# Kernel optimization log

Measured on AMD Instinct MI355X. Metric: run time of the kernel, lower is better.

Reference implementation:

```python
import jax, jax.numpy as jnp
import numpy as np

B, S, D = 8, 2048, 512
EPS = 1e-6
ROPE_THETA = 10000.0


def setup_inputs() -> dict:
    key = jax.random.key(0)
    ks = jax.random.split(key, 8)
    scale = 0.02
    return {
        "x": jax.random.normal(ks[0], (B, S, D), dtype=jnp.float32),
        "conv_w": jax.random.normal(ks[1], (D, D, 3), dtype=jnp.float32) * scale,
        "conv_b": jnp.zeros((D,), dtype=jnp.float32),
        "pre_g": jnp.ones((D,), dtype=jnp.float32),
        "q_g": jnp.ones((D,), dtype=jnp.float32),
        "k_g": jnp.ones((D,), dtype=jnp.float32),
        "Wq": jax.random.normal(ks[2], (D, D), dtype=jnp.float32) * scale,
        "Wk": jax.random.normal(ks[3], (D, D), dtype=jnp.float32) * scale,
        "Wv": jax.random.normal(ks[4], (D, D), dtype=jnp.float32) * scale,
    }


def _rmsnorm(x, g, eps=EPS):
    ms = jnp.mean(jnp.square(x), axis=-1, keepdims=True)
    return x * jax.lax.rsqrt(ms + eps) * g


def _rope_tables(seq_len, head_dim, dtype=jnp.float32):
    inv = 1.0 / (ROPE_THETA ** (jnp.arange(0, head_dim, 2, dtype=dtype) / head_dim))
    freqs = jnp.arange(seq_len, dtype=dtype)[:, None] * inv[None, :]  # [S, D/2]
    return jnp.cos(freqs), jnp.sin(freqs)


def _apply_rope(x, cos, sin):
    # x: [B, S, D]; treat last dim as D/2 complex pairs (interleaved real/imag)
    b, s, d = x.shape
    xr = x.reshape(b, s, d // 2, 2)
    x0, x1 = xr[..., 0], xr[..., 1]
    c = cos[None, :, :]
    sn = sin[None, :, :]
    o0 = x0 * c - x1 * sn
    o1 = x0 * sn + x1 * c
    return jnp.stack([o0, o1], axis=-1).reshape(b, s, d)


def reference(x, conv_w, conv_b, pre_g, q_g, k_g, Wq, Wk, Wv):
    b, s, d = x.shape
    # Conv1d over sequence axis (kernel 3, padding 1)
    xc = jnp.transpose(x, (0, 2, 1))  # [B, D, S]
    xc = jax.lax.conv_general_dilated(
        xc, conv_w, window_strides=(1,), padding=[(1, 1)],
        dimension_numbers=("NCH", "OIH", "NCH"))
    xc = xc + conv_b[None, :, None]
    x_norm = _rmsnorm(jnp.transpose(xc, (0, 2, 1)), pre_g)  # [B, S, D]

    q = _rmsnorm(jnp.einsum("bsd,ed->bse", x_norm, Wq), q_g)
    k = _rmsnorm(jnp.einsum("bsd,ed->bse", x_norm, Wk), k_g)
    v = jnp.einsum("bsd,ed->bse", x_norm, Wv)

    cos, sin = _rope_tables(s, d, x.dtype)
    q = _apply_rope(q, cos, sin)
    k = _apply_rope(k, cos, sin)

    scores = jnp.einsum("bqd,bkd->bqk", q, k) / jnp.sqrt(jnp.asarray(d, x.dtype))
    w = jax.nn.softmax(scores, axis=-1)  # dropout is identity in eval mode
    attended = jnp.einsum("bqk,bkd->bqd", w, v)
    out = x + attended
    return out.mean(axis=1)  # [B, D]
```

## Files before the change

### kernel.cpp

```cpp
#include <hip/hip_runtime.h>
#include <math.h>

#define BB 8
#define SS 2048
#define DDIM 512
#define KC 1536
#define EPSV 1e-6f
#define SCALE 0.044194173824159216f
#define LDP 40

typedef unsigned short ushort_t;
using short8 = __attribute__((ext_vector_type(8))) short;
using f32x4  = __attribute__((ext_vector_type(4))) float;

__device__ inline unsigned short f2bf(float f) {
    union { float f; unsigned int u; } v; v.f = f;
    unsigned int r = v.u + 0x7FFFu + ((v.u >> 16) & 1u);
    return (unsigned short)(r >> 16);
}
__device__ inline unsigned int packbf(float a, float b) {
    return (unsigned int)f2bf(a) | ((unsigned int)f2bf(b) << 16);
}
__device__ inline float bf2f(unsigned short s) {
    union { unsigned int u; float f; } v; v.u = ((unsigned int)s) << 16; return v.f;
}
__device__ inline short8 ldfrag(const ushort_t* s, int row, int ko) {
    return *reinterpret_cast<const short8*>(&s[row * LDP + ko]);
}

__global__ __launch_bounds__(256) void kx_cast(const float* __restrict__ x, ushort_t* __restrict__ xbf)
{
    int i = (blockIdx.x * 256 + threadIdx.x) * 4;
    float4 v = *reinterpret_cast<const float4*>(&x[i]);
    unsigned int lo = packbf(v.x, v.y), hi = packbf(v.z, v.w);
    *reinterpret_cast<uint2*>(&xbf[i]) = make_uint2(lo, hi);
}

__global__ __launch_bounds__(256) void k0_prep(
    const float* __restrict__ conv_w, const float* __restrict__ Wq,
    const float* __restrict__ Wk, const float* __restrict__ Wv,
    ushort_t* __restrict__ wcat, ushort_t* __restrict__ wqkv)
{
    int idx = blockIdx.x * 256 + threadIdx.x;
    {
        int o = idx / KC, kk = idx - o * KC;
        int t = kk >> 9, i = kk & 511;
        wcat[idx] = f2bf(conv_w[(size_t)o * KC + i * 3 + t]);
    }
    {
        int n = idx >> 9, d = idx & 511;
        const float* src = (n < 512) ? &Wq[(size_t)n * DDIM + d]
                         : (n < 1024) ? &Wk[(size_t)(n - 512) * DDIM + d]
                         : &Wv[(size_t)(n - 1024) * DDIM + d];
        wqkv[idx] = f2bf(*src);
    }
}

__global__ __launch_bounds__(256, 4) void k1b_conv(
    const ushort_t* __restrict__ xbf, const ushort_t* __restrict__ wcat,
    const float* __restrict__ conv_b, ushort_t* __restrict__ ybf, float* __restrict__ rs)
{
    __shared__ ushort_t As[128 * LDP];
    __shared__ ushort_t Bs[128 * LDP];
    const int t = threadIdx.x;
    const int lane = t & 63, w = t >> 6;
    const int lm = lane & 15, lq = lane >> 4;
    const int wm = w >> 1, wn = w & 1;
    const int srow = t >> 2, scol = (t & 3) * 8;
    const int s0 = blockIdx.x * 128;
    const int n0 = blockIdx.y * 128;
    const int b  = blockIdx.z;
    const ushort_t* Ag = xbf + (size_t)b * SS * DDIM;
    const ushort_t* Bg = wcat + (size_t)n0 * KC;

    f32x4 acc[4][4];
    #pragma unroll
    for (int i = 0; i < 4; i++)
        #pragma unroll
        for (int j = 0; j < 4; j++) acc[i][j] = (f32x4){0.f, 0.f, 0.f, 0.f};

    const uint4 z4 = make_uint4(0, 0, 0, 0);
    #define LOADA(dc, ro, dst) { \
        int s_ = s0 + srow + (ro) + ((dc) >> 4) - 1; \
        int ic_ = (((dc) & 15) << 5) + scol; \
        dst = (s_ >= 0 && s_ < SS) ? *reinterpret_cast<const uint4*>(&Ag[(size_t)s_ * DDIM + ic_]) : z4; }

    uint4 ra0, ra1, rb0, rb1;
    LOADA(0, 0, ra0); LOADA(0, 64, ra1);
    rb0 = *reinterpret_cast<const uint4*>(&Bg[(size_t)srow * KC + scol]);
    rb1 = *reinterpret_cast<const uint4*>(&Bg[(size_t)(srow + 64) * KC + scol]);

    for (int dc = 0; dc < 48; dc++) {
        *reinterpret_cast<uint4*>(&As[srow * LDP + scol]) = ra0;
        *reinterpret_cast<uint4*>(&As[(srow + 64) * LDP + scol]) = ra1;
        *reinterpret_cast<uint4*>(&Bs[srow * LDP + scol]) = rb0;
        *reinterpret_cast<uint4*>(&Bs[(srow + 64) * LDP + scol]) = rb1;
        __syncthreads();
        if (dc < 47) {
            LOADA(dc + 1, 0, ra0); LOADA(dc + 1, 64, ra1);
            int c = (dc + 1) * 32 + scol;
            rb0 = *reinterpret_cast<const uint4*>(&Bg[(size_t)srow * KC + c]);
            rb1 = *reinterpret_cast<const uint4*>(&Bg[(size_t)(srow + 64) * KC + c]);
        }
        short8 af[4];
        #pragma unroll
        for (int mt = 0; mt < 4; mt++)
            af[mt] = ldfrag(As, wm * 64 + mt * 16 + lm, lq * 8);
        #pragma unroll
        for (int nt = 0; nt < 4; nt++) {
            short8 bfv = ldfrag(Bs, wn * 64 + nt * 16 + lm, lq * 8);
            #pragma unroll
            for (int mt = 0; mt < 4; mt++)
                acc[mt][nt] = __builtin_amdgcn_mfma_f32_16x16x32_bf16(af[mt], bfv, acc[mt][nt], 0, 0, 0);
        }
        __syncthreads();
    }
    #undef LOADA

    const int rbase = s0 + wm * 64;
    const int cbase = n0 + wn * 64;
    ushort_t* yb = ybf + (size_t)b * SS * DDIM;
    float* rsb = rs + (size_t)b * SS;
    float bias[4];
    #pragma unroll
    for (int nt = 0; nt < 4; nt++) bias[nt] = conv_b[cbase + nt * 16 + lm];
    #pragma unroll
    for (int mt = 0; mt < 4; mt++) {
        float pr[4] = {0.f, 0.f, 0.f, 0.f};
        #pragma unroll
        for (int nt = 0; nt < 4; nt++) {
            #pragma unroll
            for (int r = 0; r < 4; r++) {
                float val = acc[mt][nt][r] + bias[nt];
                yb[(size_t)(rbase + mt * 16 + lq * 4 + r) * DDIM + cbase + nt * 16 + lm] = f2bf(val);
                pr[r] = fmaf(val, val, pr[r]);
            }
        }
        #pragma unroll
        for (int r = 0; r < 4; r++) {
            float p = pr[r];
            p += __shfl_xor(p, 1, 64); p += __shfl_xor(p, 2, 64);
            p += __shfl_xor(p, 4, 64); p += __shfl_xor(p, 8, 64);
            if (lm == 0) atomicAdd(&rsb[rbase + mt * 16 + lq * 4 + r], p);
        }
    }
}

__global__ __launch_bounds__(256) void k1n_norm(
    const ushort_t* __restrict__ ybf, const float* __restrict__ rs,
    const float* __restrict__ pre_g, ushort_t* __restrict__ xnbf)
{
    const int t = threadIdx.x;
    const int b = blockIdx.y;
    const int r0 = blockIdx.x * 8;
    float2 pg = *reinterpret_cast<const float2*>(&pre_g[2 * t]);
    for (int r = 0; r < 8; r++) {
        size_t row = (size_t)b * SS + r0 + r;
        float inv = rsqrtf(rs[row] * (1.0f / DDIM) + EPSV);
        unsigned int yv = *reinterpret_cast<const unsigned int*>(&ybf[row * DDIM + 2 * t]);
        float v0 = bf2f((ushort_t)(yv & 0xFFFF)), v1 = bf2f((ushort_t)(yv >> 16));
        *reinterpret_cast<unsigned int*>(&xnbf[row * DDIM + 2 * t]) =
            packbf(v0 * inv * pg.x, v1 * inv * pg.y);
    }
}

__global__ __launch_bounds__(256, 4) void k1c_qkv(
    const ushort_t* __restrict__ xnbf, const ushort_t* __restrict__ wqkv,
    ushort_t* __restrict__ qraw, ushort_t* __restrict__ kraw, ushort_t* __restrict__ vb,
    float* __restrict__ rq, float* __restrict__ rk)
{
    __shared__ ushort_t As[128 * LDP];
    __shared__ ushort_t Bs[128 * LDP];
    const int t = threadIdx.x;
    const int lane = t & 63, w = t >> 6;
    const int lm = lane & 15, lq = lane >> 4;
    const int wm = w >> 1, wn = w & 1;
    const int srow = t >> 2, scol = (t & 3) * 8;
    const int s0 = blockIdx.x * 128;
    const int n0 = blockIdx.y * 128;
    const int b  = blockIdx.z;
    const ushort_t* Ag = xnbf + (size_t)b * SS * DDIM;
    const ushort_t* Bg = wqkv + (size_t)n0 * DDIM;

    f32x4 acc[4][4];
    #pragma unroll
    for (int i = 0; i < 4; i++)
        #pragma unroll
        for (int j = 0; j < 4; j++) acc[i][j] = (f32x4){0.f, 0.f, 0.f, 0.f};

    uint4 ra0 = *reinterpret_cast<const uint4*>(&Ag[(size_t)(s0 + srow) * DDIM + scol]);
    uint4 ra1 = *reinterpret_cast<const uint4*>(&Ag[(size_t)(s0 + srow + 64) * DDIM + scol]);
    uint4 rb0 = *reinterpret_cast<const uint4*>(&Bg[(size_t)srow * DDIM + scol]);
    uint4 rb1 = *reinterpret_cast<const uint4*>(&Bg[(size_t)(srow + 64) * DDIM + scol]);

    for (int dc = 0; dc < 16; dc++) {
        *reinterpret_cast<uint4*>(&As[srow * LDP + scol]) = ra0;
        *reinterpret_cast<uint4*>(&As[(srow + 64) * LDP + scol]) = ra1;
        *reinterpret_cast<uint4*>(&Bs[srow * LDP + scol]) = rb0;
        *reinterpret_cast<uint4*>(&Bs[(srow + 64) * LDP + scol]) = rb1;
        __syncthreads();
        if (dc < 15) {
            int c = (dc + 1) * 32 + scol;
            ra0 = *reinterpret_cast<const uint4*>(&Ag[(size_t)(s0 + srow) * DDIM + c]);
            ra1 = *reinterpret_cast<const uint4*>(&Ag[(size_t)(s0 + srow + 64) * DDIM + c]);
            rb0 = *reinterpret_cast<const uint4*>(&Bg[(size_t)srow * DDIM + c]);
            rb1 = *reinterpret_cast<const uint4*>(&Bg[(size_t)(srow + 64) * DDIM + c]);
        }
        short8 af[4];
        #pragma unroll
        for (int mt = 0; mt < 4; mt++)
            af[mt] = ldfrag(As, wm * 64 + mt * 16 + lm, lq * 8);
        #pragma unroll
        for (int nt = 0; nt < 4; nt++) {
            short8 bfv = ldfrag(Bs, wn * 64 + nt * 16 + lm, lq * 8);
            #pragma unroll
            for (int mt = 0; mt < 4; mt++)
                acc[mt][nt] = __builtin_amdgcn_mfma_f32_16x16x32_bf16(af[mt], bfv, acc[mt][nt], 0, 0, 0);
        }
        __syncthreads();
    }

    const int which = blockIdx.y >> 2;
    const int rbase = s0 + wm * 64;
    const int cbase = ((blockIdx.y & 3) * 128) + wn * 64;
    if (which == 2) {
        ushort_t* vbb = vb + (size_t)b * SS * DDIM;
        #pragma unroll
        for (int mt = 0; mt < 4; mt++)
            #pragma unroll
            for (int nt = 0; nt < 4; nt++)
                #pragma unroll
                for (int r = 0; r < 4; r++)
                    vbb[(size_t)(rbase + mt * 16 + lq * 4 + r) * DDIM + cbase + nt * 16 + lm] =
                        f2bf(acc[mt][nt][r]);
    } else {
        ushort_t* db = (which ? kraw : qraw) + (size_t)b * SS * DDIM;
        float* rb = (which ? rk : rq) + (size_t)b * SS;
        #pragma unroll
        for (int mt = 0; mt < 4; mt++) {
            float pr[4] = {0.f, 0.f, 0.f, 0.f};
            #pragma unroll
            for (int nt = 0; nt < 4; nt++) {
                #pragma unroll
                for (int r = 0; r < 4; r++) {
                    float val = acc[mt][nt][r];
                    db[(size_t)(rbase + mt * 16 + lq * 4 + r) * DDIM + cbase + nt * 16 + lm] = f2bf(val);
                    pr[r] = fmaf(val, val, pr[r]);
                }
            }
            #pragma unroll
            for (int r = 0; r < 4; r++) {
                float p = pr[r];
                p += __shfl_xor(p, 1, 64); p += __shfl_xor(p, 2, 64);
                p += __shfl_xor(p, 4, 64); p += __shfl_xor(p, 8, 64);
                if (lm == 0) atomicAdd(&rb[rbase + mt * 16 + lq * 4 + r], p);
            }
        }
    }
}

__global__ __launch_bounds__(256) void k1d_rope(
    ushort_t* q_io, ushort_t* k_io,
    const float* __restrict__ rq, const float* __restrict__ rk,
    const float* __restrict__ q_g, const float* __restrict__ k_g)
{
    const int t = threadIdx.x;
    const int b = blockIdx.y;
    const int r0 = blockIdx.x * 8;
    const int c0 = 2 * t;
    float qg0 = q_g[c0], qg1 = q_g[c0 + 1];
    float kg0 = k_g[c0], kg1 = k_g[c0 + 1];
    float invf = (float)pow(10000.0, -(double)c0 / (double)DDIM);
    for (int r = 0; r < 8; r++) {
        int srow = r0 + r;
        size_t rowi = (size_t)b * SS + srow;
        float iq = rsqrtf(rq[rowi] * (1.0f / DDIM) + EPSV);
        float ik = rsqrtf(rk[rowi] * (1.0f / DDIM) + EPSV);
        size_t off = rowi * DDIM + c0;
        unsigned int qv = *reinterpret_cast<const unsigned int*>(&q_io[off]);
        unsigned int kv = *reinterpret_cast<const unsigned int*>(&k_io[off]);
        float q0 = bf2f((ushort_t)(qv & 0xFFFF)) * iq * qg0;
        float q1 = bf2f((ushort_t)(qv >> 16)) * iq * qg1;
        float k0v = bf2f((ushort_t)(kv & 0xFFFF)) * ik * kg0;
        float k1v = bf2f((ushort_t)(kv >> 16)) * ik * kg1;
        float ang = (float)srow * invf, sn, cs;
        sincosf(ang, &sn, &cs);
        *reinterpret_cast<unsigned int*>(&q_io[off]) = packbf(q0 * cs - q1 * sn, q0 * sn + q1 * cs);
        *reinterpret_cast<unsigned int*>(&k_io[off]) = packbf(k0v * cs - k1v * sn, k0v * sn + k1v * cs);
    }
}

__global__ __launch_bounds__(256, 4) void k2a_rowsum(
    const ushort_t* __restrict__ qb, const ushort_t* __restrict__ kb,
    ushort_t* __restrict__ P, float* __restrict__ l)
{
    __shared__ ushort_t As[128 * LDP];
    __shared__ ushort_t Bs[128 * LDP];
    const int t = threadIdx.x;
    const int lane = t & 63, w = t >> 6;
    const int lm = lane & 15, lq = lane >> 4;
    const int wm = w >> 1, wn = w & 1;
    const int srow = t >> 2, scol = (t & 3) * 8;
    const int b  = blockIdx.x;
    const int qt = blockIdx.y;
    const int kt = blockIdx.z;

    const ushort_t* Ag = qb + ((size_t)b * SS + qt * 128) * DDIM;
    const ushort_t* Bg = kb + ((size_t)b * SS + kt * 128) * DDIM;

    f32x4 acc[4][4];
    #pragma unroll
    for (int i = 0; i < 4; i++)
        #pragma unroll
        for (int j = 0; j < 4; j++) acc[i][j] = (f32x4){0.f, 0.f, 0.f, 0.f};

    uint4 ra0 = *reinterpret_cast<const uint4*>(&Ag[(size_t)srow * DDIM + scol]);
    uint4 ra1 = *reinterpret_cast<const uint4*>(&Ag[(size_t)(srow + 64) * DDIM + scol]);
    uint4 rb0 = *reinterpret_cast<const uint4*>(&Bg[(size_t)srow * DDIM + scol]);
    uint4 rb1 = *reinterpret_cast<const uint4*>(&Bg[(size_t)(srow + 64) * DDIM + scol]);

    for (int dc = 0; dc < 16; dc++) {
        *reinterpret_cast<uint4*>(&As[srow * LDP + scol]) = ra0;
        *reinterpret_cast<uint4*>(&As[(srow + 64) * LDP + scol]) = ra1;
        *reinterpret_cast<uint4*>(&Bs[srow * LDP + scol]) = rb0;
        *reinterpret_cast<uint4*>(&Bs[(srow + 64) * LDP + scol]) = rb1;
        __syncthreads();
        if (dc < 15) {
            int off = (dc + 1) * 32 + scol;
            ra0 = *reinterpret_cast<const uint4*>(&Ag[(size_t)srow * DDIM + off]);
            ra1 = *reinterpret_cast<const uint4*>(&Ag[(size_t)(srow + 64) * DDIM + off]);
            rb0 = *reinterpret_cast<const uint4*>(&Bg[(size_t)srow * DDIM + off]);
            rb1 = *reinterpret_cast<const uint4*>(&Bg[(size_t)(srow + 64) * DDIM + off]);
        }
        short8 af[4];
        #pragma unroll
        for (int mt = 0; mt < 4; mt++)
            af[mt] = ldfrag(As, wm * 64 + mt * 16 + lm, lq * 8);
        #pragma unroll
        for (int nt = 0; nt < 4; nt++) {
            short8 bfv = ldfrag(Bs, wn * 64 + nt * 16 + lm, lq * 8);
            #pragma unroll
            for (int mt = 0; mt < 4; mt++)
                acc[mt][nt] = __builtin_amdgcn_mfma_f32_16x16x32_bf16(af[mt], bfv, acc[mt][nt], 0, 0, 0);
        }
        __syncthreads();
    }

    const int rbase = qt * 128 + wm * 64;
    const int cbase = kt * 128 + wn * 64;
    ushort_t* Pb = P + (size_t)b * SS * SS;
    float* lrow = l + (size_t)b * SS;
    #pragma unroll
    for (int mt = 0; mt < 4; mt++) {
        #pragma unroll
        for (int r = 0; r < 4; r++) {
            const int row = rbase + mt * 16 + lq * 4 + r;
            float rowp = 0.f;
            #pragma unroll
            for (int nt = 0; nt < 4; nt++) {
                float e = __expf(acc[mt][nt][r] * SCALE);
                Pb[(size_t)row * SS + cbase + nt * 16 + lm] = f2bf(e);
                rowp += e;
            }
            float p = rowp;
            p += __shfl_xor(p, 1, 64); p += __shfl_xor(p, 2, 64);
            p += __shfl_xor(p, 4, 64); p += __shfl_xor(p, 8, 64);
            if (lm == 0) atomicAdd(&lrow[row], p);
        }
    }
}

__global__ __launch_bounds__(256) void k2c_colred(
    const ushort_t* __restrict__ P, const float* __restrict__ l,
    float* __restrict__ cw)
{
    const int t = threadIdx.x;
    const int b = blockIdx.z;
    const int k0 = blockIdx.x * 1024 + t * 4;
    const int q0 = blockIdx.y * 128;
    const ushort_t* Pb = P + ((size_t)b * SS + q0) * SS;
    const float* lb = l + (size_t)b * SS + q0;
    float a0 = 0.f, a1 = 0.f, a2 = 0.f, a3 = 0.f;
    for (int q = 0; q < 128; q++) {
        float rl = 1.0f / lb[q];
        uint2 pp = *reinterpret_cast<const uint2*>(&Pb[(size_t)q * SS + k0]);
        a0 = fmaf(bf2f((ushort_t)(pp.x & 0xFFFF)), rl, a0);
        a1 = fmaf(bf2f((ushort_t)(pp.x >> 16)), rl, a1);
        a2 = fmaf(bf2f((ushort_t)(pp.y & 0xFFFF)), rl, a2);
        a3 = fmaf(bf2f((ushort_t)(pp.y >> 16)), rl, a3);
    }
    atomicAdd(&cw[(size_t)b * SS + k0], a0);
    atomicAdd(&cw[(size_t)b * SS + k0 + 1], a1);
    atomicAdd(&cw[(size_t)b * SS + k0 + 2], a2);
    atomicAdd(&cw[(size_t)b * SS + k0 + 3], a3);
}

__global__ __launch_bounds__(256) void k4_out(
    const float* __restrict__ x, const ushort_t* __restrict__ v,
    const float* __restrict__ cwv, float* __restrict__ out)
{
    const int b = blockIdx.x, c = blockIdx.y;
    const int t = threadIdx.x;
    const int srow0 = c * (SS / 16);
    const float* xb    = x + ((size_t)b * SS + srow0) * DDIM;
    const ushort_t* vb = v + ((size_t)b * SS + srow0) * DDIM;
    const float* cwb   = cwv + (size_t)b * SS + srow0;
    float a0 = 0.f, a1 = 0.f;
    for (int r = 0; r < SS / 16; r++) {
        float w = cwb[r];
        a0 += xb[(size_t)r * DDIM + t]       + w * bf2f(vb[(size_t)r * DDIM + t]);
        a1 += xb[(size_t)r * DDIM + t + 256] + w * bf2f(vb[(size_t)r * DDIM + t + 256]);
    }
    atomicAdd(&out[b * DDIM + t],       a0 * (1.0f / SS));
    atomicAdd(&out[b * DDIM + t + 256], a1 * (1.0f / SS));
}

extern "C" void kernel_launch(void* const* d_in, const int* in_sizes, int n_in,
                              void* d_out, int out_size, void* d_ws, size_t ws_size,
                              hipStream_t stream)
{
    const float* x      = (const float*)d_in[0];
    const float* conv_w = (const float*)d_in[1];
    const float* conv_b = (const float*)d_in[2];
    const float* pre_g  = (const float*)d_in[3];
    const float* q_g    = (const float*)d_in[4];
    const float* k_g    = (const float*)d_in[5];
    const float* Wq     = (const float*)d_in[6];
    const float* Wk     = (const float*)d_in[7];
    const float* Wv     = (const float*)d_in[8];
    float* out          = (float*)d_out;

    const size_t NTOK = (size_t)BB * SS * DDIM;
    char* p = (char*)d_ws;
    ushort_t* xbf = (ushort_t*)p; p += NTOK * 2;
    ushort_t* ybf = (ushort_t*)p; p += NTOK * 2;
    ushort_t* xn  = (ushort_t*)p; p += NTOK * 2;
                         p += NTOK * 2;
    ushort_t* qio = (ushort_t*)p; p += NTOK * 2;
    ushort_t* kio = (ushort_t*)p; p += NTOK * 2;
    ushort_t* vb  = (ushort_t*)p; p += NTOK * 2;
    ushort_t* wcat = (ushort_t*)p; p += (size_t)DDIM * KC * 2;
    ushort_t* wqkv = (ushort_t*)p; p += (size_t)KC * DDIM * 2;
    float* rs   = (float*)p; p += (size_t)BB * SS * 4;
    float* rq   = (float*)p; p += (size_t)BB * SS * 4;
    float* rk   = (float*)p; p += (size_t)BB * SS * 4;
    float* lbuf = (float*)p; p += (size_t)BB * SS * 4;
    float* cwb  = (float*)p; p += (size_t)BB * SS * 4;

    ushort_t* Pbuf = xbf;

    (void)hipMemsetAsync(d_out, 0, (size_t)out_size * sizeof(float), stream);
    (void)hipMemsetAsync(rs, 0, (size_t)BB * SS * 5 * sizeof(float), stream);

    kx_cast<<<dim3((unsigned)(NTOK / 1024)), 256, 0, stream>>>(x, xbf);
    k0_prep<<<dim3(DDIM * KC / 256), 256, 0, stream>>>(conv_w, Wq, Wk, Wv, wcat, wqkv);
    k1b_conv<<<dim3(SS / 128, 4, BB), 256, 0, stream>>>(xbf, wcat, conv_b, ybf, rs);
    k1n_norm<<<dim3(SS / 8, BB), 256, 0, stream>>>(ybf, rs, pre_g, xn);
    k1c_qkv<<<dim3(SS / 128, 12, BB), 256, 0, stream>>>(xn, wqkv, qio, kio, vb, rq, rk);
    k1d_rope<<<dim3(SS / 8, BB), 256, 0, stream>>>(qio, kio, rq, rk, q_g, k_g);
    k2a_rowsum<<<dim3(BB, SS / 128, SS / 128), 256, 0, stream>>>(qio, kio, Pbuf, lbuf);
    k2c_colred<<<dim3(SS / 1024, SS / 128, BB), 256, 0, stream>>>(Pbuf, lbuf, cwb);
    k4_out<<<dim3(BB, 16), 256, 0, stream>>>(x, vb, cwb, out);
}
```

Measured before the change: 287.8 us.

## Use global_load_lds direct-to-LDS loads with fragment-ordered tiles and padded conv input

```diff
diff --git a/kernel.cpp b/kernel.cpp
--- a/kernel.cpp
+++ b/kernel.cpp
@@ -3,11 +3,11 @@
 
 #define BB 8
 #define SS 2048
+#define SP 2050
 #define DDIM 512
 #define KC 1536
 #define EPSV 1e-6f
 #define SCALE 0.044194173824159216f
-#define LDP 40
 
 typedef unsigned short ushort_t;
 using short8 = __attribute__((ext_vector_type(8))) short;
@@ -24,16 +24,29 @@
 __device__ inline float bf2f(unsigned short s) {
     union { unsigned int u; float f; } v; v.u = ((unsigned int)s) << 16; return v.f;
 }
-__device__ inline short8 ldfrag(const ushort_t* s, int row, int ko) {
-    return *reinterpret_cast<const short8*>(&s[row * LDP + ko]);
-}
-
-__global__ __launch_bounds__(256) void kx_cast(const float* __restrict__ x, ushort_t* __restrict__ xbf)
-{
-    int i = (blockIdx.x * 256 + threadIdx.x) * 4;
-    float4 v = *reinterpret_cast<const float4*>(&x[i]);
-    unsigned int lo = packbf(v.x, v.y), hi = packbf(v.z, v.w);
-    *reinterpret_cast<uint2*>(&xbf[i]) = make_uint2(lo, hi);
+
+typedef const __attribute__((address_space(1))) void gv_t;
+typedef __attribute__((address_space(3))) void sv_t;
+__device__ inline void gll16(const void* g, void* s) {
+    __builtin_amdgcn_global_load_lds((gv_t*)g, (sv_t*)s, 16, 0, 0);
+}
+
+__device__ inline short8 ldfragFO(const ushort_t* s, int rg, int lane) {
+    return *reinterpret_cast<const short8*>(&s[rg * 512 + lane * 8]);
+}
+
+__global__ __launch_bounds__(256) void kx_cast(const float* __restrict__ x, ushort_t* __restrict__ xpad)
+{
+    int c = blockIdx.x * 256 + threadIdx.x;
+    int r = c >> 7, ci = (c & 127) * 4;
+    int b = r / SP, rb = r - b * SP;
+    size_t dsti = ((size_t)b * SP + rb) * DDIM + ci;
+    if (rb == 0 || rb == SP - 1) {
+        *reinterpret_cast<uint2*>(&xpad[dsti]) = make_uint2(0u, 0u);
+    } else {
+        const float4 v = *reinterpret_cast<const float4*>(&x[((size_t)b * SS + rb - 1) * DDIM + ci]);
+        *reinterpret_cast<uint2*>(&xpad[dsti]) = make_uint2(packbf(v.x, v.y), packbf(v.z, v.w));
+    }
 }
 
 __global__ __launch_bounds__(256) void k0_prep(
@@ -57,20 +70,19 @@
 }
 
 __global__ __launch_bounds__(256, 4) void k1b_conv(
-    const ushort_t* __restrict__ xbf, const ushort_t* __restrict__ wcat,
+    const ushort_t* __restrict__ xpad, const ushort_t* __restrict__ wcat,
     const float* __restrict__ conv_b, ushort_t* __restrict__ ybf, float* __restrict__ rs)
 {
-    __shared__ ushort_t As[128 * LDP];
-    __shared__ ushort_t Bs[128 * LDP];
+    __shared__ ushort_t As[4096];
+    __shared__ ushort_t Bs[4096];
     const int t = threadIdx.x;
     const int lane = t & 63, w = t >> 6;
     const int lm = lane & 15, lq = lane >> 4;
     const int wm = w >> 1, wn = w & 1;
-    const int srow = t >> 2, scol = (t & 3) * 8;
     const int s0 = blockIdx.x * 128;
     const int n0 = blockIdx.y * 128;
     const int b  = blockIdx.z;
-    const ushort_t* Ag = xbf + (size_t)b * SS * DDIM;
+    const ushort_t* Ab = xpad + (size_t)b * SP * DDIM;
     const ushort_t* Bg = wcat + (size_t)n0 * KC;
 
     f32x4 acc[4][4];
@@ -79,43 +91,29 @@
         #pragma unroll
         for (int j = 0; j < 4; j++) acc[i][j] = (f32x4){0.f, 0.f, 0.f, 0.f};
 
-    const uint4 z4 = make_uint4(0, 0, 0, 0);
-    #define LOADA(dc, ro, dst) { \
-        int s_ = s0 + srow + (ro) + ((dc) >> 4) - 1; \
-        int ic_ = (((dc) & 15) << 5) + scol; \
-        dst = (s_ >= 0 && s_ < SS) ? *reinterpret_cast<const uint4*>(&Ag[(size_t)s_ * DDIM + ic_]) : z4; }
-
-    uint4 ra0, ra1, rb0, rb1;
-    LOADA(0, 0, ra0); LOADA(0, 64, ra1);
-    rb0 = *reinterpret_cast<const uint4*>(&Bg[(size_t)srow * KC + scol]);
-    rb1 = *reinterpret_cast<const uint4*>(&Bg[(size_t)(srow + 64) * KC + scol]);
+    const int ar0 = w * 16 + lm, ar1 = (w + 4) * 16 + lm;
+    const int ac  = lq * 8;
 
     for (int dc = 0; dc < 48; dc++) {
-        *reinterpret_cast<uint4*>(&As[srow * LDP + scol]) = ra0;
-        *reinterpret_cast<uint4*>(&As[(srow + 64) * LDP + scol]) = ra1;
-        *reinterpret_cast<uint4*>(&Bs[srow * LDP + scol]) = rb0;
-        *reinterpret_cast<uint4*>(&Bs[(srow + 64) * LDP + scol]) = rb1;
-        __syncthreads();
-        if (dc < 47) {
-            LOADA(dc + 1, 0, ra0); LOADA(dc + 1, 64, ra1);
-            int c = (dc + 1) * 32 + scol;
-            rb0 = *reinterpret_cast<const uint4*>(&Bg[(size_t)srow * KC + c]);
-            rb1 = *reinterpret_cast<const uint4*>(&Bg[(size_t)(srow + 64) * KC + c]);
-        }
+        const int tg = dc >> 4, ko = (dc & 15) * 32;
+        gll16(&Ab[(size_t)(s0 + ar0 + tg) * DDIM + ko + ac], &As[w * 512]);
+        gll16(&Ab[(size_t)(s0 + ar1 + tg) * DDIM + ko + ac], &As[(w + 4) * 512]);
+        gll16(&Bg[(size_t)ar0 * KC + dc * 32 + ac], &Bs[w * 512]);
+        gll16(&Bg[(size_t)ar1 * KC + dc * 32 + ac], &Bs[(w + 4) * 512]);
+        __syncthreads();
         short8 af[4];
         #pragma unroll
         for (int mt = 0; mt < 4; mt++)
-            af[mt] = ldfrag(As, wm * 64 + mt * 16 + lm, lq * 8);
+            af[mt] = ldfragFO(As, wm * 4 + mt, lane);
         #pragma unroll
         for (int nt = 0; nt < 4; nt++) {
-            short8 bfv = ldfrag(Bs, wn * 64 + nt * 16 + lm, lq * 8);
+            short8 bfv = ldfragFO(Bs, wn * 4 + nt, lane);
             #pragma unroll
             for (int mt = 0; mt < 4; mt++)
                 acc[mt][nt] = __builtin_amdgcn_mfma_f32_16x16x32_bf16(af[mt], bfv, acc[mt][nt], 0, 0, 0);
         }
         __syncthreads();
     }
-    #undef LOADA
 
     const int rbase = s0 + wm * 64;
     const int cbase = n0 + wn * 64;
@@ -169,17 +167,16 @@
     ushort_t* __restrict__ qraw, ushort_t* __restrict__ kraw, ushort_t* __restrict__ vb,
     float* __restrict__ rq, float* __restrict__ rk)
 {
-    __shared__ ushort_t As[128 * LDP];
-    __shared__ ushort_t Bs[128 * LDP];
+    __shared__ ushort_t As[4096];
+    __shared__ ushort_t Bs[4096];
     const int t = threadIdx.x;
     const int lane = t & 63, w = t >> 6;
     const int lm = lane & 15, lq = lane >> 4;
     const int wm = w >> 1, wn = w & 1;
-    const int srow = t >> 2, scol = (t & 3) * 8;
     const int s0 = blockIdx.x * 128;
     const int n0 = blockIdx.y * 128;
     const int b  = blockIdx.z;
-    const ushort_t* Ag = xnbf + (size_t)b * SS * DDIM;
+    const ushort_t* Ag = xnbf + ((size_t)b * SS + s0) * DDIM;
     const ushort_t* Bg = wqkv + (size_t)n0 * DDIM;
 
     f32x4 acc[4][4];
@@ -188,31 +185,23 @@
         #pragma unroll
         for (int j = 0; j < 4; j++) acc[i][j] = (f32x4){0.f, 0.f, 0.f, 0.f};
 
-    uint4 ra0 = *reinterpret_cast<const uint4*>(&Ag[(size_t)(s0 + srow) * DDIM + scol]);
-    uint4 ra1 = *reinterpret_cast<const uint4*>(&Ag[(size_t)(s0 + srow + 64) * DDIM + scol]);
-    uint4 rb0 = *reinterpret_cast<const uint4*>(&Bg[(size_t)srow * DDIM + scol]);
-    uint4 rb1 = *reinterpret_cast<const uint4*>(&Bg[(size_t)(srow + 64) * DDIM + scol]);
+    const int ar0 = w * 16 + lm, ar1 = (w + 4) * 16 + lm;
+    const int ac  = lq * 8;
 
     for (int dc = 0; dc < 16; dc++) {
-        *reinterpret_cast<uint4*>(&As[srow * LDP + scol]) = ra0;
-        *reinterpret_cast<uint4*>(&As[(srow + 64) * LDP + scol]) = ra1;
-        *reinterpret_cast<uint4*>(&Bs[srow * LDP + scol]) = rb0;
-        *reinterpret_cast<uint4*>(&Bs[(srow + 64) * LDP + scol]) = rb1;
-        __syncthreads();
-        if (dc < 15) {
-            int c = (dc + 1) * 32 + scol;
-            ra0 = *reinterpret_cast<const uint4*>(&Ag[(size_t)(s0 + srow) * DDIM + c]);
-            ra1 = *reinterpret_cast<const uint4*>(&Ag[(size_t)(s0 + srow + 64) * DDIM + c]);
-            rb0 = *reinterpret_cast<const uint4*>(&Bg[(size_t)srow * DDIM + c]);
-            rb1 = *reinterpret_cast<const uint4*>(&Bg[(size_t)(srow + 64) * DDIM + c]);
-        }
+        const int ko = dc * 32 + ac;
+        gll16(&Ag[(size_t)ar0 * DDIM + ko], &As[w * 512]);
+        gll16(&Ag[(size_t)ar1 * DDIM + ko], &As[(w + 4) * 512]);
+        gll16(&Bg[(size_t)ar0 * DDIM + ko], &Bs[w * 512]);
+        gll16(&Bg[(size_t)ar1 * DDIM + ko], &Bs[(w + 4) * 512]);
+        __syncthreads();
         short8 af[4];
         #pragma unroll
         for (int mt = 0; mt < 4; mt++)
-            af[mt] = ldfrag(As, wm * 64 + mt * 16 + lm, lq * 8);
+            af[mt] = ldfragFO(As, wm * 4 + mt, lane);
         #pragma unroll
         for (int nt = 0; nt < 4; nt++) {
-            short8 bfv = ldfrag(Bs, wn * 64 + nt * 16 + lm, lq * 8);
+            short8 bfv = ldfragFO(Bs, wn * 4 + nt, lane);
             #pragma unroll
             for (int mt = 0; mt < 4; mt++)
                 acc[mt][nt] = __builtin_amdgcn_mfma_f32_16x16x32_bf16(af[mt], bfv, acc[mt][nt], 0, 0, 0);
@@ -294,13 +283,12 @@
     const ushort_t* __restrict__ qb, const ushort_t* __restrict__ kb,
     ushort_t* __restrict__ P, float* __restrict__ l)
 {
-    __shared__ ushort_t As[128 * LDP];
-    __shared__ ushort_t Bs[128 * LDP];
+    __shared__ ushort_t As[4096];
+    __shared__ ushort_t Bs[4096];
     const int t = threadIdx.x;
     const int lane = t & 63, w = t >> 6;
     const int lm = lane & 15, lq = lane >> 4;
     const int wm = w >> 1, wn = w & 1;
-    const int srow = t >> 2, scol = (t & 3) * 8;
     const int b  = blockIdx.x;
     const int qt = blockIdx.y;
     const int kt = blockIdx.z;
@@ -314,31 +302,23 @@
         #pragma unroll
         for (int j = 0; j < 4; j++) acc[i][j] = (f32x4){0.f, 0.f, 0.f, 0.f};
 
-    uint4 ra0 = *reinterpret_cast<const uint4*>(&Ag[(size_t)srow * DDIM + scol]);
-    uint4 ra1 = *reinterpret_cast<const uint4*>(&Ag[(size_t)(srow + 64) * DDIM + scol]);
-    uint4 rb0 = *reinterpret_cast<const uint4*>(&Bg[(size_t)srow * DDIM + scol]);
-    uint4 rb1 = *reinterpret_cast<const uint4*>(&Bg[(size_t)(srow + 64) * DDIM + scol]);
+    const int ar0 = w * 16 + lm, ar1 = (w + 4) * 16 + lm;
+    const int ac  = lq * 8;
 
     for (int dc = 0; dc < 16; dc++) {
-        *reinterpret_cast<uint4*>(&As[srow * LDP + scol]) = ra0;
-        *reinterpret_cast<uint4*>(&As[(srow + 64) * LDP + scol]) = ra1;
-        *reinterpret_cast<uint4*>(&Bs[srow * LDP + scol]) = rb0;
-        *reinterpret_cast<uint4*>(&Bs[(srow + 64) * LDP + scol]) = rb1;
-        __syncthreads();
-        if (dc < 15) {
-            int off = (dc + 1) * 32 + scol;
-            ra0 = *reinterpret_cast<const uint4*>(&Ag[(size_t)srow * DDIM + off]);
-            ra1 = *reinterpret_cast<const uint4*>(&Ag[(size_t)(srow + 64) * DDIM + off]);
-            rb0 = *reinterpret_cast<const uint4*>(&Bg[(size_t)srow * DDIM + off]);
-            rb1 = *reinterpret_cast<const uint4*>(&Bg[(size_t)(srow + 64) * DDIM + off]);
-        }
+        const int ko = dc * 32 + ac;
+        gll16(&Ag[(size_t)ar0 * DDIM + ko], &As[w * 512]);
+        gll16(&Ag[(size_t)ar1 * DDIM + ko], &As[(w + 4) * 512]);
+        gll16(&Bg[(size_t)ar0 * DDIM + ko], &Bs[w * 512]);
+        gll16(&Bg[(size_t)ar1 * DDIM + ko], &Bs[(w + 4) * 512]);
+        __syncthreads();
         short8 af[4];
         #pragma unroll
         for (int mt = 0; mt < 4; mt++)
-            af[mt] = ldfrag(As, wm * 64 + mt * 16 + lm, lq * 8);
+            af[mt] = ldfragFO(As, wm * 4 + mt, lane);
         #pragma unroll
         for (int nt = 0; nt < 4; nt++) {
-            short8 bfv = ldfrag(Bs, wn * 64 + nt * 16 + lm, lq * 8);
+            short8 bfv = ldfragFO(Bs, wn * 4 + nt, lane);
             #pragma unroll
             for (int mt = 0; mt < 4; mt++)
                 acc[mt][nt] = __builtin_amdgcn_mfma_f32_16x16x32_bf16(af[mt], bfv, acc[mt][nt], 0, 0, 0);
@@ -431,11 +411,14 @@
     float* out          = (float*)d_out;
 
     const size_t NTOK = (size_t)BB * SS * DDIM;
+    const size_t NPAD = (size_t)BB * SP * DDIM;
+    const size_t PBYTES = (size_t)BB * SS * SS * 2;
     char* p = (char*)d_ws;
-    ushort_t* xbf = (ushort_t*)p; p += NTOK * 2;
-    ushort_t* ybf = (ushort_t*)p; p += NTOK * 2;
-    ushort_t* xn  = (ushort_t*)p; p += NTOK * 2;
-                         p += NTOK * 2;
+    char* pregion = p;
+    ushort_t* xpad = (ushort_t*)p; p += NPAD * 2;
+    ushort_t* ybf  = (ushort_t*)p; p += NTOK * 2;
+    ushort_t* xn   = (ushort_t*)p; p += NTOK * 2;
+    p = pregion + PBYTES;
     ushort_t* qio = (ushort_t*)p; p += NTOK * 2;
     ushort_t* kio = (ushort_t*)p; p += NTOK * 2;
     ushort_t* vb  = (ushort_t*)p; p += NTOK * 2;
@@ -447,14 +430,14 @@
     float* lbuf = (float*)p; p += (size_t)BB * SS * 4;
     float* cwb  = (float*)p; p += (size_t)BB * SS * 4;
 
-    ushort_t* Pbuf = xbf;
+    ushort_t* Pbuf = (ushort_t*)pregion;
 
     (void)hipMemsetAsync(d_out, 0, (size_t)out_size * sizeof(float), stream);
     (void)hipMemsetAsync(rs, 0, (size_t)BB * SS * 5 * sizeof(float), stream);
 
-    kx_cast<<<dim3((unsigned)(NTOK / 1024)), 256, 0, stream>>>(x, xbf);
+    kx_cast<<<dim3((unsigned)(NPAD / 1024)), 256, 0, stream>>>(x, xpad);
     k0_prep<<<dim3(DDIM * KC / 256), 256, 0, stream>>>(conv_w, Wq, Wk, Wv, wcat, wqkv);
-    k1b_conv<<<dim3(SS / 128, 4, BB), 256, 0, stream>>>(xbf, wcat, conv_b, ybf, rs);
+    k1b_conv<<<dim3(SS / 128, 4, BB), 256, 0, stream>>>(xpad, wcat, conv_b, ybf, rs);
     k1n_norm<<<dim3(SS / 8, BB), 256, 0, stream>>>(ybf, rs, pre_g, xn);
     k1c_qkv<<<dim3(SS / 128, 12, BB), 256, 0, stream>>>(xn, wqkv, qio, kio, vb, rq, rk);
     k1d_rope<<<dim3(SS / 8, BB), 256, 0, stream>>>(qio, kio, rq, rk, q_g, k_g);
```

New measurement: 345.8 us. 1.2x slower.
